# Kernel tuning notes

Measured on AMD Instinct MI355X. Metric: run time of the kernel, lower is better.

## Reference

```python
import jax, jax.numpy as jnp
import numpy as np
import math

B, L, D, H = 2, 2048, 512, 8
DH = D // H  # 64
MAX_SEQ = 2048


def setup_inputs() -> dict:
    key = jax.random.key(0)
    ks = jax.random.split(key, 9)
    rn = lambda k, sh: jax.random.normal(k, sh, dtype=jnp.float32)
    w_scale = 0.02
    # causal mask: 1 where attention is disallowed (upper triangle)
    causal = jnp.triu(jnp.ones((L, L), jnp.float32), k=1)[None, None]
    return {
        "q_in": rn(ks[0], (B, L, D)),
        "k_in": rn(ks[1], (B, L, D)),
        "v_in": rn(ks[2], (B, L, D)),
        "mask": causal,
        "Wq": rn(ks[3], (D, D)) * w_scale,
        "bq": jnp.zeros((D,), jnp.float32),
        "Wk": rn(ks[4], (D, D)) * w_scale,
        "bk": jnp.zeros((D,), jnp.float32),
        "Wv": rn(ks[5], (D, D)) * w_scale,
        "bv": jnp.zeros((D,), jnp.float32),
        "Wfc": rn(ks[6], (D, D)) * w_scale,
        "bfc": jnp.zeros((D,), jnp.float32),
        "E": rn(ks[7], (MAX_SEQ, DH)),  # relative position embedding (non-trainable buffer)
    }


def _heads(x, W, b):
    # [B,L,D] -> [B,H,L,DH]
    y = x @ W + b
    return y.reshape(x.shape[0], x.shape[1], H, DH).transpose(0, 2, 1, 3)


def _qe_mask(len_q):
    # keep[l, m] = (m >= len_q - 1 - l); zeros out invalid relative offsets
    rows = jnp.arange(len_q)[:, None]
    cols = jnp.arange(len_q)[None, :]
    return (cols >= (len_q - 1 - rows)).astype(jnp.float32)


def _skew(QE):
    # Music-Transformer skewing: [B,H,L,M] -> pad left on last dim ->
    # reshape swapping last two dims -> drop first row => Srel [B,H,M,L]
    b, h, l, m = QE.shape
    padded = jnp.pad(QE, ((0, 0), (0, 0), (0, 0), (1, 0)))  # [b,h,l,m+1]
    reshaped = padded.reshape(b, h, m + 1, l)
    return reshaped[:, :, 1:, :]  # [b,h,m,l]


def reference(q_in, k_in, v_in, mask, Wq, bq, Wk, bk, Wv, bv, Wfc, bfc, E):
    q = _heads(q_in, Wq, bq)  # [B,H,L,DH]
    k = _heads(k_in, Wk, bk)
    v = _heads(v_in, Wv, bv)
    len_q = q.shape[2]
    # left embedding slice: E[max(0, MAX_SEQ - len_q):]
    e = E[max(0, MAX_SEQ - len_q):, :]  # [M, DH], M == len_q here
    QE = jnp.einsum('bhld,md->bhlm', q, e)
    QE = QE * _qe_mask(len_q)  # broadcast [L,M] over [B,H,L,M]
    Srel = _skew(QE)  # [B,H,L,L]
    QKt = jnp.einsum('bhld,bhmd->bhlm', q, k)
    logits = (QKt + Srel) / np.sqrt(DH).astype(np.float32)
    logits = logits + mask * (-1e9)
    attn_weights = jax.nn.softmax(logits, axis=-1)
    attn = jnp.einsum('bhlm,bhmd->bhld', attn_weights, v)
    out = attn.transpose(0, 2, 1, 3).reshape(q_in.shape[0], -1, D)
    out = out @ Wfc + bfc
    return out, attn_weights
```

## Files before the change

### kernel.cpp

```cpp
#include <hip/hip_runtime.h>
#include <math.h>

#define L 2048
#define DMODEL 512
#define NH 8
#define DH 64
#define NROWS 4096

typedef __attribute__((ext_vector_type(4))) float f32x4;
typedef __attribute__((ext_vector_type(8))) short s16x8;

#define MFMA(a, b, c) __builtin_amdgcn_mfma_f32_16x16x32_bf16(a, b, c, 0, 0, 0)

static __device__ __forceinline__ ushort f2b(float f) {
    union { float f; unsigned u; } v; v.f = f;
    unsigned r = v.u + 0x7FFF + ((v.u >> 16) & 1);
    return (ushort)(r >> 16);
}
static __device__ __forceinline__ float b2f(ushort u) {
    union { unsigned u; float f; } v; v.u = ((unsigned)u) << 16;
    return v.f;
}

__global__ __launch_bounds__(256)
void cvt_bf16(const float* __restrict__ in, ushort* __restrict__ out, int n8) {
    int i = blockIdx.x * 256 + threadIdx.x;
    if (i < n8) {
        float4 a = *reinterpret_cast<const float4*>(&in[(size_t)i * 8]);
        float4 b = *reinterpret_cast<const float4*>(&in[(size_t)i * 8 + 4]);
        ushort4 o0; o0.x = f2b(a.x); o0.y = f2b(a.y); o0.z = f2b(a.z); o0.w = f2b(a.w);
        ushort4 o1; o1.x = f2b(b.x); o1.y = f2b(b.y); o1.z = f2b(b.z); o1.w = f2b(b.w);
        *reinterpret_cast<ushort4*>(&out[(size_t)i * 8]) = o0;
        *reinterpret_cast<ushort4*>(&out[(size_t)i * 8 + 4]) = o1;
    }
}

__global__ __launch_bounds__(256)
void transpose_w(const float* __restrict__ W0, const float* __restrict__ W1,
                 const float* __restrict__ W2, const float* __restrict__ W3,
                 ushort* __restrict__ T0, ushort* __restrict__ T1,
                 ushort* __restrict__ T2, ushort* __restrict__ T3) {
    const int z = blockIdx.z;
    const float* W = z == 0 ? W0 : (z == 1 ? W1 : (z == 2 ? W2 : W3));
    ushort* T = z == 0 ? T0 : (z == 1 ? T1 : (z == 2 ? T2 : T3));
    __shared__ float Ls[64][65];
    const int tid = threadIdx.x;
    const int k0 = blockIdx.y * 64, n0 = blockIdx.x * 64;
    #pragma unroll
    for (int i = 0; i < 4; ++i) {
        int kk = (tid >> 4) + i * 16, n4 = (tid & 15) * 4;
        float4 v = *reinterpret_cast<const float4*>(&W[(size_t)(k0 + kk) * 512 + n0 + n4]);
        Ls[kk][n4] = v.x; Ls[kk][n4 + 1] = v.y; Ls[kk][n4 + 2] = v.z; Ls[kk][n4 + 3] = v.w;
    }
    __syncthreads();
    #pragma unroll
    for (int i = 0; i < 4; ++i) {
        int nn = (tid >> 4) + i * 16, k4 = (tid & 15) * 4;
        ushort4 o;
        o.x = f2b(Ls[k4 + 0][nn]); o.y = f2b(Ls[k4 + 1][nn]);
        o.z = f2b(Ls[k4 + 2][nn]); o.w = f2b(Ls[k4 + 3][nn]);
        *reinterpret_cast<ushort4*>(&T[(size_t)(n0 + nn) * 512 + k0 + k4]) = o;
    }
}

__global__ __launch_bounds__(256)
void gemm_bf16(const void* __restrict__ A0, const void* __restrict__ A1,
               const void* __restrict__ A2,
               const ushort* __restrict__ W0, const ushort* __restrict__ W1,
               const ushort* __restrict__ W2,
               const float* __restrict__ b0, const float* __restrict__ b1,
               const float* __restrict__ b2,
               void* o0, void* o1, void* o2, int a_f32, int modes) {
    const int z = blockIdx.z;
    const void* A   = z == 0 ? A0 : (z == 1 ? A1 : A2);
    const ushort* Wt = z == 0 ? W0 : (z == 1 ? W1 : W2);
    const float* bias = z == 0 ? b0 : (z == 1 ? b1 : b2);
    void* outp = z == 0 ? o0 : (z == 1 ? o1 : o2);
    const int mode = (modes >> (4 * z)) & 15;

    __shared__ ushort As[128][40];
    __shared__ ushort Bs[64][40];
    const int tid = threadIdx.x;
    const int w = tid >> 6, lane = tid & 63, g = lane >> 4, c = lane & 15;
    const int m0 = blockIdx.y * 128, n0 = blockIdx.x * 64;

    f32x4 acc[2][4];
    #pragma unroll
    for (int rs = 0; rs < 2; ++rs)
        #pragma unroll
        for (int cs = 0; cs < 4; ++cs) acc[rs][cs] = (f32x4){0.f, 0.f, 0.f, 0.f};

    float bsv[4];
    #pragma unroll
    for (int cs = 0; cs < 4; ++cs) bsv[cs] = bias[n0 + 16 * cs + c];

    for (int k0 = 0; k0 < 512; k0 += 32) {
        {
            int row = tid >> 1, kh = (tid & 1) * 16;
            if (a_f32) {
                const float* p = (const float*)A + (size_t)(m0 + row) * 512 + k0 + kh;
                ushort tmp[16];
                #pragma unroll
                for (int q4 = 0; q4 < 4; ++q4) {
                    float4 f = *reinterpret_cast<const float4*>(p + q4 * 4);
                    tmp[q4 * 4 + 0] = f2b(f.x); tmp[q4 * 4 + 1] = f2b(f.y);
                    tmp[q4 * 4 + 2] = f2b(f.z); tmp[q4 * 4 + 3] = f2b(f.w);
                }
                *reinterpret_cast<uint4*>(&As[row][kh]) = *reinterpret_cast<uint4*>(&tmp[0]);
                *reinterpret_cast<uint4*>(&As[row][kh + 8]) = *reinterpret_cast<uint4*>(&tmp[8]);
            } else {
                const ushort* p = (const ushort*)A + (size_t)(m0 + row) * 512 + k0 + kh;
                uint4 x0 = *reinterpret_cast<const uint4*>(p);
                uint4 x1 = *reinterpret_cast<const uint4*>(p + 8);
                *reinterpret_cast<uint4*>(&As[row][kh]) = x0;
                *reinterpret_cast<uint4*>(&As[row][kh + 8]) = x1;
            }
        }
        {
            int n = tid >> 2, kh = (tid & 3) * 8;
            uint4 x = *reinterpret_cast<const uint4*>(&Wt[(size_t)(n0 + n) * 512 + k0 + kh]);
            *reinterpret_cast<uint4*>(&Bs[n][kh]) = x;
        }
        __syncthreads();
        s16x8 af[2], bf[4];
        #pragma unroll
        for (int rs = 0; rs < 2; ++rs)
            af[rs] = *reinterpret_cast<const s16x8*>(&As[32 * w + 16 * rs + c][8 * g]);
        #pragma unroll
        for (int cs = 0; cs < 4; ++cs)
            bf[cs] = *reinterpret_cast<const s16x8*>(&Bs[16 * cs + c][8 * g]);
        #pragma unroll
        for (int rs = 0; rs < 2; ++rs)
            #pragma unroll
            for (int cs = 0; cs < 4; ++cs)
                acc[rs][cs] = MFMA(af[rs], bf[cs], acc[rs][cs]);
        __syncthreads();
    }
    #pragma unroll
    for (int rs = 0; rs < 2; ++rs)
        #pragma unroll
        for (int cs = 0; cs < 4; ++cs)
            #pragma unroll
            for (int r = 0; r < 4; ++r) {
                int row = m0 + 32 * w + 16 * rs + 4 * g + r;
                int n = n0 + 16 * cs + c;
                float v = acc[rs][cs][r] + bsv[cs];
                int bb = row >> 11, l = row & 2047, hh = n >> 6, dh = n & 63;
                if (mode == 0) {
                    ((float*)outp)[(size_t)row * 512 + n] = v;
                } else if (mode == 1) {
                    ((ushort*)outp)[(((size_t)bb * NH + hh) * L + l) * DH + dh] = f2b(v);
                } else {
                    ((ushort*)outp)[(((size_t)bb * NH + hh) * DH + dh) * L + l] = f2b(v);
                }
            }
}

__global__ __launch_bounds__(256, 4)
void attn(const ushort* __restrict__ qws, const ushort* __restrict__ kws,
          const ushort* __restrict__ vtg, const ushort* __restrict__ Ebf,
          ushort* __restrict__ pcomp, ushort* __restrict__ ows,
          float* __restrict__ linvg) {
    __shared__ ushort PwAll[4][32 * 40];
    __shared__ float lred[4][32];
    __shared__ float linvs[32];

    const int tid = threadIdx.x;
    const int w = tid >> 6, lane = tid & 63, g = lane >> 4, c = lane & 15;
    const int bid = blockIdx.x;
    const int bh = bid & 15;
    const int ib = 63 - (bid >> 4);
    const int b = bh >> 3, h = bh & 7;
    const int i0 = ib * 32;
    const int nt = ib + 1;

    const ushort* qb = qws + (size_t)bh * L * DH;
    const ushort* kb = kws + (size_t)bh * L * DH;
    const ushort* vt = vtg + (size_t)bh * DH * L;
    ushort* pblk = pcomp + ((size_t)bh * 2080 + (size_t)ib * (ib + 1) / 2) * 1024;

    ushort* Pw = &PwAll[w][0];

    s16x8 aq[2][2];
    #pragma unroll
    for (int rs = 0; rs < 2; ++rs)
        #pragma unroll
        for (int ks = 0; ks < 2; ++ks)
            aq[rs][ks] = *reinterpret_cast<const s16x8*>(
                qb + (size_t)(i0 + 16 * rs + c) * DH + 32 * ks + 8 * g);

    float lsum[2][4] = {};
    f32x4 O[2][4];
    #pragma unroll
    for (int rs = 0; rs < 2; ++rs)
        #pragma unroll
        for (int cs = 0; cs < 4; ++cs) O[rs][cs] = (f32x4){0.f, 0.f, 0.f, 0.f};

    for (int t = w; t < nt; t += 4) {
        const int j0 = t * 32;
        const int rbase = L - 32 - i0 + j0;
        f32x4 TT[4][2];
        #pragma unroll
        for (int ct = 0; ct < 4; ++ct) {
            int rg = rbase + 16 * ct + c;
            rg = rg > L - 1 ? L - 1 : rg;
            s16x8 be0 = *reinterpret_cast<const s16x8*>(Ebf + (size_t)rg * DH + 8 * g);
            s16x8 be1 = *reinterpret_cast<const s16x8*>(Ebf + (size_t)rg * DH + 32 + 8 * g);
            #pragma unroll
            for (int rs = 0; rs < 2; ++rs) {
                f32x4 x = {0.f, 0.f, 0.f, 0.f};
                x = MFMA(aq[rs][0], be0, x);
                x = MFMA(aq[rs][1], be1, x);
                TT[ct][rs] = x;
            }
        }
        float rel[2][2][4];
        #pragma unroll
        for (int r = 0; r < 4; ++r) {
            const int u = c - 4 * g - r;
            const int src = (lane & 48) | ((15 + u) & 15);
            const bool hi = (u >= 1);
            #pragma unroll
            for (int rs = 0; rs < 2; ++rs)
                #pragma unroll
                for (int jh = 0; jh < 2; ++jh) {
                    const int b0 = jh - rs + 1;
                    float va = __shfl(TT[b0][rs][r], src);
                    float vb = __shfl(TT[b0 + 1][rs][r], src);
                    rel[rs][jh][r] = hi ? vb : va;
                }
        }
        s16x8 bk[2][2];
        #pragma unroll
        for (int jh = 0; jh < 2; ++jh)
            #pragma unroll
            for (int ks = 0; ks < 2; ++ks)
                bk[jh][ks] = *reinterpret_cast<const s16x8*>(
                    kb + (size_t)(j0 + 16 * jh + c) * DH + 32 * ks + 8 * g);
        #pragma unroll
        for (int rs = 0; rs < 2; ++rs)
            #pragma unroll
            for (int jh = 0; jh < 2; ++jh) {
                f32x4 x = {0.f, 0.f, 0.f, 0.f};
                x = MFMA(aq[rs][0], bk[jh][0], x);
                x = MFMA(aq[rs][1], bk[jh][1], x);
                #pragma unroll
                for (int r = 0; r < 4; ++r) {
                    const int il = 16 * rs + 4 * g + r;
                    const int jl = 16 * jh + c;
                    float s = (x[r] + rel[rs][jh][r]) * 0.125f;
                    float p = (j0 + jl <= i0 + il) ? __expf(s) : 0.0f;
                    lsum[rs][r] += p;
                    Pw[il * 40 + jl] = f2b(p);
                }
            }
        {
            const int row = lane >> 1, cb = (lane & 1) * 16;
            uint4 x0 = *reinterpret_cast<const uint4*>(&Pw[row * 40 + cb]);
            uint4 x1 = *reinterpret_cast<const uint4*>(&Pw[row * 40 + cb + 8]);
            ushort* dst = pblk + (size_t)t * 1024 + lane * 16;
            *reinterpret_cast<uint4*>(dst) = x0;
            *reinterpret_cast<uint4*>(dst + 8) = x1;
        }
        s16x8 pa[2];
        #pragma unroll
        for (int rs2 = 0; rs2 < 2; ++rs2)
            pa[rs2] = *reinterpret_cast<const s16x8*>(&Pw[(16 * rs2 + c) * 40 + 8 * g]);
        #pragma unroll
        for (int cs = 0; cs < 4; ++cs) {
            s16x8 vtb = *reinterpret_cast<const s16x8*>(
                vt + (size_t)(16 * cs + c) * L + j0 + 8 * g);
            #pragma unroll
            for (int rs2 = 0; rs2 < 2; ++rs2)
                O[rs2][cs] = MFMA(pa[rs2], vtb, O[rs2][cs]);
        }
    }

    #pragma unroll
    for (int rs = 0; rs < 2; ++rs)
        #pragma unroll
        for (int r = 0; r < 4; ++r) {
            float s = lsum[rs][r];
            s += __shfl_xor(s, 1); s += __shfl_xor(s, 2);
            s += __shfl_xor(s, 4); s += __shfl_xor(s, 8);
            if (c == 0) lred[w][16 * rs + 4 * g + r] = s;
        }
    __syncthreads();
    if (tid < 32) {
        float l = lred[0][tid] + lred[1][tid] + lred[2][tid] + lred[3][tid];
        float inv = 1.0f / l;
        linvs[tid] = inv;
        linvg[(size_t)bh * L + i0 + tid] = inv;
    }
    __syncthreads();

    float (*Obuf)[68] = reinterpret_cast<float(*)[68]>(&PwAll[0][0]);
    #pragma unroll
    for (int ww = 0; ww < 4; ++ww) {
        if (w == ww) {
            #pragma unroll
            for (int rs2 = 0; rs2 < 2; ++rs2)
                #pragma unroll
                for (int cs = 0; cs < 4; ++cs)
                    #pragma unroll
                    for (int r = 0; r < 4; ++r) {
                        const int row = 16 * rs2 + 4 * g + r;
                        const int col = 16 * cs + c;
                        if (ww == 0) Obuf[row][col] = O[rs2][cs][r];
                        else         Obuf[row][col] += O[rs2][cs][r];
                    }
        }
        __syncthreads();
    }
    {
        const int i = tid >> 3, d8 = (tid & 7) * 8;
        const float inv = linvs[i];
        ushort o[8];
        #pragma unroll
        for (int e = 0; e < 8; ++e) o[e] = f2b(Obuf[i][d8 + e] * inv);
        *reinterpret_cast<uint4*>(
            &ows[((size_t)b * L + i0 + i) * DMODEL + h * DH + d8]) =
            *reinterpret_cast<const uint4*>(&o[0]);
    }
}

__global__ __launch_bounds__(256)
void rescale(const ushort* __restrict__ pcomp, const float* __restrict__ linvg,
             float* __restrict__ attnw) {
    const int blk = blockIdx.x;
    const int bh = blk >> 11, i = blk & 2047;
    const int ib = i >> 5, r = i & 31;
    const float inv = linvg[((size_t)bh << 11) + i];
    const ushort* rowb = pcomp + ((size_t)bh * 2080 + (size_t)ib * (ib + 1) / 2) * 1024 + r * 32;
    float* dst = attnw + (((size_t)bh << 11) + i) * 2048;
    const int col0 = threadIdx.x * 8;
    f32x4 o0 = {0.f, 0.f, 0.f, 0.f}, o1 = {0.f, 0.f, 0.f, 0.f};
    if (col0 <= i) {
        const int t = col0 >> 5;
        const ushort* src = rowb + (size_t)t * 1024 + (col0 & 31);
        ushort4 u0 = *reinterpret_cast<const ushort4*>(src);
        ushort4 u1 = *reinterpret_cast<const ushort4*>(src + 4);
        o0[0] = (col0 + 0 <= i) ? b2f(u0.x) * inv : 0.f;
        o0[1] = (col0 + 1 <= i) ? b2f(u0.y) * inv : 0.f;
        o0[2] = (col0 + 2 <= i) ? b2f(u0.z) * inv : 0.f;
        o0[3] = (col0 + 3 <= i) ? b2f(u0.w) * inv : 0.f;
        o1[0] = (col0 + 4 <= i) ? b2f(u1.x) * inv : 0.f;
        o1[1] = (col0 + 5 <= i) ? b2f(u1.y) * inv : 0.f;
        o1[2] = (col0 + 6 <= i) ? b2f(u1.z) * inv : 0.f;
        o1[3] = (col0 + 7 <= i) ? b2f(u1.w) * inv : 0.f;
    }
    __builtin_nontemporal_store(o0, reinterpret_cast<f32x4*>(dst + col0));
    __builtin_nontemporal_store(o1, reinterpret_cast<f32x4*>(dst + col0 + 4));
}

extern "C" void kernel_launch(void* const* d_in, const int* in_sizes, int n_in,
                              void* d_out, int out_size, void* d_ws, size_t ws_size,
                              hipStream_t stream) {
    const float* q_in = (const float*)d_in[0];
    const float* k_in = (const float*)d_in[1];
    const float* v_in = (const float*)d_in[2];
    const float* Wq  = (const float*)d_in[4];
    const float* bq  = (const float*)d_in[5];
    const float* Wk  = (const float*)d_in[6];
    const float* bk  = (const float*)d_in[7];
    const float* Wv  = (const float*)d_in[8];
    const float* bv  = (const float*)d_in[9];
    const float* Wfc = (const float*)d_in[10];
    const float* bfc = (const float*)d_in[11];
    const float* E   = (const float*)d_in[12];

    float* out0  = (float*)d_out;
    float* attnw = out0 + (size_t)2 * L * DMODEL;

    const size_t NA = (size_t)NROWS * DMODEL;
    ushort* ws = (ushort*)d_ws;
    ushort* Ebf  = ws;
    ushort* Wqt  = Ebf + (size_t)L * DH;
    ushort* Wkt  = Wqt + 262144;
    ushort* Wvt  = Wkt + 262144;
    ushort* Wfct = Wvt + 262144;
    ushort* qws  = Wfct + 262144;
    ushort* kws  = qws + NA;
    ushort* vtg  = kws + NA;
    ushort* ows  = vtg + NA;
    float*  linvg = (float*)(ows + NA);
    ushort* pcomp = (ushort*)(linvg + 32768);

    cvt_bf16<<<dim3(64), 256, 0, stream>>>(E, Ebf, (int)(L * DH / 8));
    transpose_w<<<dim3(8, 8, 4), 256, 0, stream>>>(Wq, Wk, Wv, Wfc, Wqt, Wkt, Wvt, Wfct);
    gemm_bf16<<<dim3(8, 32, 3), 256, 0, stream>>>(q_in, k_in, v_in, Wqt, Wkt, Wvt,
                                                  bq, bk, bv, qws, kws, vtg,
                                                  1, 0x211);
    attn<<<dim3(1024), 256, 0, stream>>>(qws, kws, vtg, Ebf, pcomp, ows, linvg);
    rescale<<<dim3(32768), 256, 0, stream>>>(pcomp, linvg, attnw);
    gemm_bf16<<<dim3(8, 32, 1), 256, 0, stream>>>(ows, ows, ows, Wfct, Wfct, Wfct,
                                                  bfc, bfc, bfc, out0, out0, out0,
                                                  0, 0x0);
}
```

Baseline: 237.9 us.

## Split attention key range across two blocks and write unnormalized probabilities directly

```diff
diff --git a/kernel.cpp b/kernel.cpp
--- a/kernel.cpp
+++ b/kernel.cpp
@@ -16,10 +16,6 @@
     union { float f; unsigned u; } v; v.f = f;
     unsigned r = v.u + 0x7FFF + ((v.u >> 16) & 1);
     return (ushort)(r >> 16);
-}
-static __device__ __forceinline__ float b2f(ushort u) {
-    union { unsigned u; float f; } v; v.u = ((unsigned)u) << 16;
-    return v.f;
 }
 
 __global__ __launch_bounds__(256)
@@ -33,6 +29,11 @@
         *reinterpret_cast<ushort4*>(&out[(size_t)i * 8]) = o0;
         *reinterpret_cast<ushort4*>(&out[(size_t)i * 8 + 4]) = o1;
     }
+}
+
+__global__ __launch_bounds__(256)
+void zerol(float* __restrict__ lg) {
+    lg[blockIdx.x * 256 + threadIdx.x] = 0.0f;
 }
 
 __global__ __launch_bounds__(256)
@@ -70,7 +71,9 @@
                const ushort* __restrict__ W2,
                const float* __restrict__ b0, const float* __restrict__ b1,
                const float* __restrict__ b2,
-               void* o0, void* o1, void* o2, int a_f32, int modes) {
+               void* o0, void* o1, void* o2,
+               const float* __restrict__ ogB, const float* __restrict__ lgp,
+               int a_f32, int modes) {
     const int z = blockIdx.z;
     const void* A   = z == 0 ? A0 : (z == 1 ? A1 : A2);
     const ushort* Wt = z == 0 ? W0 : (z == 1 ? W1 : W2);
@@ -97,7 +100,7 @@
     for (int k0 = 0; k0 < 512; k0 += 32) {
         {
             int row = tid >> 1, kh = (tid & 1) * 16;
-            if (a_f32) {
+            if (a_f32 == 1) {
                 const float* p = (const float*)A + (size_t)(m0 + row) * 512 + k0 + kh;
                 ushort tmp[16];
                 #pragma unroll
@@ -105,6 +108,25 @@
                     float4 f = *reinterpret_cast<const float4*>(p + q4 * 4);
                     tmp[q4 * 4 + 0] = f2b(f.x); tmp[q4 * 4 + 1] = f2b(f.y);
                     tmp[q4 * 4 + 2] = f2b(f.z); tmp[q4 * 4 + 3] = f2b(f.w);
+                }
+                *reinterpret_cast<uint4*>(&As[row][kh]) = *reinterpret_cast<uint4*>(&tmp[0]);
+                *reinterpret_cast<uint4*>(&As[row][kh + 8]) = *reinterpret_cast<uint4*>(&tmp[8]);
+            } else if (a_f32 == 2) {
+                const size_t idx = (size_t)(m0 + row) * 512 + k0 + kh;
+                const float* p0 = (const float*)A + idx;
+                const float* p1 = ogB + idx;
+                const int bb = (m0 + row) >> 11, l = (m0 + row) & 2047;
+                const int head = (k0 + kh) >> 6;
+                const float inv = 1.0f / lgp[(((size_t)bb * NH + head) << 11) + l];
+                ushort tmp[16];
+                #pragma unroll
+                for (int q4 = 0; q4 < 4; ++q4) {
+                    float4 f = *reinterpret_cast<const float4*>(p0 + q4 * 4);
+                    float4 f1 = *reinterpret_cast<const float4*>(p1 + q4 * 4);
+                    tmp[q4 * 4 + 0] = f2b((f.x + f1.x) * inv);
+                    tmp[q4 * 4 + 1] = f2b((f.y + f1.y) * inv);
+                    tmp[q4 * 4 + 2] = f2b((f.z + f1.z) * inv);
+                    tmp[q4 * 4 + 3] = f2b((f.w + f1.w) * inv);
                 }
                 *reinterpret_cast<uint4*>(&As[row][kh]) = *reinterpret_cast<uint4*>(&tmp[0]);
                 *reinterpret_cast<uint4*>(&As[row][kh + 8]) = *reinterpret_cast<uint4*>(&tmp[8]);
@@ -156,28 +178,36 @@
             }
 }
 
-__global__ __launch_bounds__(256, 4)
+__global__ __launch_bounds__(256, 6)
 void attn(const ushort* __restrict__ qws, const ushort* __restrict__ kws,
           const ushort* __restrict__ vtg, const ushort* __restrict__ Ebf,
-          ushort* __restrict__ pcomp, ushort* __restrict__ ows,
-          float* __restrict__ linvg) {
+          float* __restrict__ attnw, float* __restrict__ og0,
+          float* __restrict__ og1, float* __restrict__ lg) {
     __shared__ ushort PwAll[4][32 * 40];
+    __shared__ float Obuf[32][68];
     __shared__ float lred[4][32];
-    __shared__ float linvs[32];
 
     const int tid = threadIdx.x;
     const int w = tid >> 6, lane = tid & 63, g = lane >> 4, c = lane & 15;
     const int bid = blockIdx.x;
-    const int bh = bid & 15;
-    const int ib = 63 - (bid >> 4);
+    const int ib = 63 - (bid >> 5);
+    const int bh = (bid >> 1) & 15;
+    const int half = bid & 1;
     const int b = bh >> 3, h = bh & 7;
     const int i0 = ib * 32;
     const int nt = ib + 1;
+    const int mid = (nt + 1) >> 1;
+    const int h0 = half ? mid : 0;
+    const int h1 = half ? nt : mid;
+    const int len = h1 - h0;
+    const int tw0 = h0 + ((len * w) >> 2);
+    const int tw1 = h0 + ((len * (w + 1)) >> 2);
 
     const ushort* qb = qws + (size_t)bh * L * DH;
     const ushort* kb = kws + (size_t)bh * L * DH;
     const ushort* vt = vtg + (size_t)bh * DH * L;
-    ushort* pblk = pcomp + ((size_t)bh * 2080 + (size_t)ib * (ib + 1) / 2) * 1024;
+    float* ab = attnw + (size_t)bh * L * L;
+    float* og = half ? og1 : og0;
 
     ushort* Pw = &PwAll[w][0];
 
@@ -196,12 +226,11 @@
         #pragma unroll
         for (int cs = 0; cs < 4; ++cs) O[rs][cs] = (f32x4){0.f, 0.f, 0.f, 0.f};
 
-    for (int t = w; t < nt; t += 4) {
-        const int j0 = t * 32;
-        const int rbase = L - 32 - i0 + j0;
-        f32x4 TT[4][2];
-        #pragma unroll
-        for (int ct = 0; ct < 4; ++ct) {
+    f32x4 TT[4][2];
+    if (tw0 < tw1) {
+        const int rbase = L - 32 - i0 + tw0 * 32;
+        #pragma unroll
+        for (int ct = 0; ct < 2; ++ct) {
             int rg = rbase + 16 * ct + c;
             rg = rg > L - 1 ? L - 1 : rg;
             s16x8 be0 = *reinterpret_cast<const s16x8*>(Ebf + (size_t)rg * DH + 8 * g);
@@ -212,6 +241,25 @@
                 x = MFMA(aq[rs][0], be0, x);
                 x = MFMA(aq[rs][1], be1, x);
                 TT[ct][rs] = x;
+            }
+        }
+    }
+
+    for (int t = tw0; t < tw1; ++t) {
+        const int j0 = t * 32;
+        const int rbase = L - 32 - i0 + j0;
+        #pragma unroll
+        for (int ct = 0; ct < 2; ++ct) {
+            int rg = rbase + 32 + 16 * ct + c;
+            rg = rg > L - 1 ? L - 1 : rg;
+            s16x8 be0 = *reinterpret_cast<const s16x8*>(Ebf + (size_t)rg * DH + 8 * g);
+            s16x8 be1 = *reinterpret_cast<const s16x8*>(Ebf + (size_t)rg * DH + 32 + 8 * g);
+            #pragma unroll
+            for (int rs = 0; rs < 2; ++rs) {
+                f32x4 x = {0.f, 0.f, 0.f, 0.f};
+                x = MFMA(aq[rs][0], be0, x);
+                x = MFMA(aq[rs][1], be1, x);
+                TT[2 + ct][rs] = x;
             }
         }
         float rel[2][2][4];
@@ -237,6 +285,7 @@
             for (int ks = 0; ks < 2; ++ks)
                 bk[jh][ks] = *reinterpret_cast<const s16x8*>(
                     kb + (size_t)(j0 + 16 * jh + c) * DH + 32 * ks + 8 * g);
+        float* prow = ab + (size_t)i0 * L + j0;
         #pragma unroll
         for (int rs = 0; rs < 2; ++rs)
             #pragma unroll
@@ -251,17 +300,10 @@
                     float s = (x[r] + rel[rs][jh][r]) * 0.125f;
                     float p = (j0 + jl <= i0 + il) ? __expf(s) : 0.0f;
                     lsum[rs][r] += p;
+                    prow[(size_t)il * L + jl] = p;
                     Pw[il * 40 + jl] = f2b(p);
                 }
             }
-        {
-            const int row = lane >> 1, cb = (lane & 1) * 16;
-            uint4 x0 = *reinterpret_cast<const uint4*>(&Pw[row * 40 + cb]);
-            uint4 x1 = *reinterpret_cast<const uint4*>(&Pw[row * 40 + cb + 8]);
-            ushort* dst = pblk + (size_t)t * 1024 + lane * 16;
-            *reinterpret_cast<uint4*>(dst) = x0;
-            *reinterpret_cast<uint4*>(dst + 8) = x1;
-        }
         s16x8 pa[2];
         #pragma unroll
         for (int rs2 = 0; rs2 < 2; ++rs2)
@@ -273,6 +315,11 @@
             #pragma unroll
             for (int rs2 = 0; rs2 < 2; ++rs2)
                 O[rs2][cs] = MFMA(pa[rs2], vtb, O[rs2][cs]);
+        }
+        #pragma unroll
+        for (int rs = 0; rs < 2; ++rs) {
+            TT[0][rs] = TT[2][rs];
+            TT[1][rs] = TT[3][rs];
         }
     }
 
@@ -286,15 +333,10 @@
             if (c == 0) lred[w][16 * rs + 4 * g + r] = s;
         }
     __syncthreads();
-    if (tid < 32) {
-        float l = lred[0][tid] + lred[1][tid] + lred[2][tid] + lred[3][tid];
-        float inv = 1.0f / l;
-        linvs[tid] = inv;
-        linvg[(size_t)bh * L + i0 + tid] = inv;
-    }
-    __syncthreads();
-
-    float (*Obuf)[68] = reinterpret_cast<float(*)[68]>(&PwAll[0][0]);
+    if (tid < 32)
+        atomicAdd(&lg[((size_t)bh << 11) + i0 + tid],
+                  lred[0][tid] + lred[1][tid] + lred[2][tid] + lred[3][tid]);
+
     #pragma unroll
     for (int ww = 0; ww < 4; ++ww) {
         if (w == ww) {
@@ -314,43 +356,42 @@
     }
     {
         const int i = tid >> 3, d8 = (tid & 7) * 8;
-        const float inv = linvs[i];
-        ushort o[8];
-        #pragma unroll
-        for (int e = 0; e < 8; ++e) o[e] = f2b(Obuf[i][d8 + e] * inv);
-        *reinterpret_cast<uint4*>(
-            &ows[((size_t)b * L + i0 + i) * DMODEL + h * DH + d8]) =
-            *reinterpret_cast<const uint4*>(&o[0]);
+        float* dst = &og[((size_t)b * L + i0 + i) * DMODEL + h * DH + d8];
+        *reinterpret_cast<float4*>(dst) = *reinterpret_cast<const float4*>(&Obuf[i][d8]);
+        *reinterpret_cast<float4*>(dst + 4) = *reinterpret_cast<const float4*>(&Obuf[i][d8 + 4]);
     }
 }
 
 __global__ __launch_bounds__(256)
-void rescale(const ushort* __restrict__ pcomp, const float* __restrict__ linvg,
-             float* __restrict__ attnw) {
+void rescale(float* __restrict__ attnw, const float* __restrict__ lg) {
     const int blk = blockIdx.x;
     const int bh = blk >> 11, i = blk & 2047;
-    const int ib = i >> 5, r = i & 31;
-    const float inv = linvg[((size_t)bh << 11) + i];
-    const ushort* rowb = pcomp + ((size_t)bh * 2080 + (size_t)ib * (ib + 1) / 2) * 1024 + r * 32;
-    float* dst = attnw + (((size_t)bh << 11) + i) * 2048;
+    const float inv = 1.0f / lg[((size_t)bh << 11) + i];
+    float* rowp = attnw + (((size_t)bh << 11) + i) * 2048;
     const int col0 = threadIdx.x * 8;
-    f32x4 o0 = {0.f, 0.f, 0.f, 0.f}, o1 = {0.f, 0.f, 0.f, 0.f};
-    if (col0 <= i) {
-        const int t = col0 >> 5;
-        const ushort* src = rowb + (size_t)t * 1024 + (col0 & 31);
-        ushort4 u0 = *reinterpret_cast<const ushort4*>(src);
-        ushort4 u1 = *reinterpret_cast<const ushort4*>(src + 4);
-        o0[0] = (col0 + 0 <= i) ? b2f(u0.x) * inv : 0.f;
-        o0[1] = (col0 + 1 <= i) ? b2f(u0.y) * inv : 0.f;
-        o0[2] = (col0 + 2 <= i) ? b2f(u0.z) * inv : 0.f;
-        o0[3] = (col0 + 3 <= i) ? b2f(u0.w) * inv : 0.f;
-        o1[0] = (col0 + 4 <= i) ? b2f(u1.x) * inv : 0.f;
-        o1[1] = (col0 + 5 <= i) ? b2f(u1.y) * inv : 0.f;
-        o1[2] = (col0 + 6 <= i) ? b2f(u1.z) * inv : 0.f;
-        o1[3] = (col0 + 7 <= i) ? b2f(u1.w) * inv : 0.f;
-    }
-    __builtin_nontemporal_store(o0, reinterpret_cast<f32x4*>(dst + col0));
-    __builtin_nontemporal_store(o1, reinterpret_cast<f32x4*>(dst + col0 + 4));
+    float4 a, b2;
+    if (col0 + 7 <= i) {
+        a  = *reinterpret_cast<const float4*>(rowp + col0);
+        b2 = *reinterpret_cast<const float4*>(rowp + col0 + 4);
+        a.x *= inv; a.y *= inv; a.z *= inv; a.w *= inv;
+        b2.x *= inv; b2.y *= inv; b2.z *= inv; b2.w *= inv;
+    } else if (col0 <= i) {
+        a  = *reinterpret_cast<const float4*>(rowp + col0);
+        b2 = *reinterpret_cast<const float4*>(rowp + col0 + 4);
+        a.x  = (col0 + 0 <= i) ? a.x  * inv : 0.f;
+        a.y  = (col0 + 1 <= i) ? a.y  * inv : 0.f;
+        a.z  = (col0 + 2 <= i) ? a.z  * inv : 0.f;
+        a.w  = (col0 + 3 <= i) ? a.w  * inv : 0.f;
+        b2.x = (col0 + 4 <= i) ? b2.x * inv : 0.f;
+        b2.y = (col0 + 5 <= i) ? b2.y * inv : 0.f;
+        b2.z = (col0 + 6 <= i) ? b2.z * inv : 0.f;
+        b2.w = (col0 + 7 <= i) ? b2.w * inv : 0.f;
+    } else {
+        a = make_float4(0.f, 0.f, 0.f, 0.f);
+        b2 = a;
+    }
+    *reinterpret_cast<float4*>(rowp + col0) = a;
+    *reinterpret_cast<float4*>(rowp + col0 + 4) = b2;
 }
 
 extern "C" void kernel_launch(void* const* d_in, const int* in_sizes, int n_in,
@@ -382,18 +423,19 @@
     ushort* qws  = Wfct + 262144;
     ushort* kws  = qws + NA;
     ushort* vtg  = kws + NA;
-    ushort* ows  = vtg + NA;
-    float*  linvg = (float*)(ows + NA);
-    ushort* pcomp = (ushort*)(linvg + 32768);
+    float*  og0  = (float*)(vtg + NA);
+    float*  og1  = og0 + NA;
+    float*  lg   = og1 + NA;
 
     cvt_bf16<<<dim3(64), 256, 0, stream>>>(E, Ebf, (int)(L * DH / 8));
     transpose_w<<<dim3(8, 8, 4), 256, 0, stream>>>(Wq, Wk, Wv, Wfc, Wqt, Wkt, Wvt, Wfct);
+    zerol<<<dim3(128), 256, 0, stream>>>(lg);
     gemm_bf16<<<dim3(8, 32, 3), 256, 0, stream>>>(q_in, k_in, v_in, Wqt, Wkt, Wvt,
                                                   bq, bk, bv, qws, kws, vtg,
-                                                  1, 0x211);
-    attn<<<dim3(1024), 256, 0, stream>>>(qws, kws, vtg, Ebf, pcomp, ows, linvg);
-    rescale<<<dim3(32768), 256, 0, stream>>>(pcomp, linvg, attnw);
-    gemm_bf16<<<dim3(8, 32, 1), 256, 0, stream>>>(ows, ows, ows, Wfct, Wfct, Wfct,
+                                                  og0, lg, 1, 0x211);
+    attn<<<dim3(2048), 256, 0, stream>>>(qws, kws, vtg, Ebf, attnw, og0, og1, lg);
+    rescale<<<dim3(32768), 256, 0, stream>>>(attnw, lg);
+    gemm_bf16<<<dim3(8, 32, 1), 256, 0, stream>>>(og0, og0, og0, Wfct, Wfct, Wfct,
                                                   bfc, bfc, bfc, out0, out0, out0,
-                                                  0, 0x0);
-}
+                                                  og1, lg, 2, 0x0);
+}
```

Result: slower. 473.2 us (+98.9%).
